# Kernel optimization log

Hardware: AMD Instinct MI355X
Metric: run time of the kernel (lower is better)

## Reference

```python
import jax, jax.numpy as jnp
import numpy as np

B, T, N, F = 4, 24, 10000, 64
E = 160000
K_STEPS = 3
HID = 128


def setup_inputs() -> dict:
    key = jax.random.key(0)
    ks = jax.random.split(key, 12)
    history = jax.random.normal(ks[0], (B, T, N, F), dtype=jnp.float32)
    horizon = jax.random.normal(ks[1], (B, 6, N, F), dtype=jnp.float32)
    edge_index = jax.random.randint(ks[2], (2, E), 0, N, dtype=jnp.int64)
    s = 1.0 / np.sqrt(F)
    W_enc = jax.random.normal(ks[3], (F, F), dtype=jnp.float32) * s
    W_hor = jax.random.normal(ks[4], (F, F), dtype=jnp.float32) * s
    b_enc = jnp.zeros((F,), dtype=jnp.float32)
    W_fc = jax.random.normal(ks[5], (F, F), dtype=jnp.float32) * s  # EventGAN.fc (no bias)
    b_gcn = jax.random.normal(ks[6], (F,), dtype=jnp.float32) * 0.01  # EventGAN.bias
    W1 = jax.random.normal(ks[7], (T * F, HID), dtype=jnp.float32) / np.sqrt(T * F)
    b1 = jnp.zeros((HID,), dtype=jnp.float32)
    W2 = jax.random.normal(ks[8], (HID, 1), dtype=jnp.float32) / np.sqrt(HID)
    b2 = jnp.zeros((1,), dtype=jnp.float32)
    return {"history": history, "horizon": horizon, "edge_index": edge_index,
            "W_enc": W_enc, "W_hor": W_hor, "b_enc": b_enc,
            "W_fc": W_fc, "b_gcn": b_gcn,
            "W1": W1, "b1": b1, "W2": W2, "b2": b2}


def _event_gan_step(h, row, col, norm, W_fc, b_gcn, n_nodes):
    # h: [B, N, F]; GCN-style normalized sum aggregation (EventGAN.forward)
    x = h @ W_fc  # fc, no bias
    msgs = norm[None, :, None] * x[:, row, :]  # [B, Etot, F] gather + scale
    agg = jax.vmap(lambda m: jax.ops.segment_sum(m, col, num_segments=n_nodes))(msgs)
    return agg + b_gcn


def reference(history, horizon, edge_index, W_enc, W_hor, b_enc, W_fc, b_gcn, W1, b1, W2, b2):
    b, t, n, f = history.shape
    # FeatureEncoder (stand-in): per-timestep linear over F mixing pooled horizon context
    hor_ctx = jnp.mean(horizon, axis=1) @ W_hor  # [B, N, F]
    x = jnp.tanh(jnp.einsum('btnf,fg->btng', history, W_enc) + hor_ctx[:, None, :, :] + b_enc)
    # spatial: k-step EventGAN propagation on last timestep's exogenous features
    h = x[:, -1, :, -f:]  # [B, N, F] (F == exogenous_features)
    row0, col0 = edge_index[0], edge_index[1]
    loops = jnp.arange(n, dtype=edge_index.dtype)
    row = jnp.concatenate([row0, loops])
    col = jnp.concatenate([col0, loops])
    deg = jax.ops.segment_sum(jnp.ones_like(col, dtype=h.dtype), col, num_segments=n)
    dinv = jnp.where(deg > 0, jax.lax.rsqrt(jnp.maximum(deg, 1.0)), 0.0)
    norm = dinv[row] * dinv[col]
    for _ in range(K_STEPS):
        h = _event_gan_step(h, row, col, norm, W_fc, b_gcn, n)
    x = x.at[:, -1, :, -f:].set(h)
    # temporal MLP (stand-in): flatten per-node time series -> scalar
    flat = x.transpose(0, 2, 1, 3).reshape(b * n, t * f)
    out = jax.nn.relu(flat @ W1 + b1) @ W2 + b2  # [B*N, 1]
    return out.reshape(b, n)
```

## Files before the change

### kernel.cpp

```cpp
#include <hip/hip_runtime.h>

constexpr int cB = 4, cT = 24, cN = 10000, cF = 64, cE = 160000, cHID = 128, cK = 3;

typedef short s16x4 __attribute__((ext_vector_type(4)));
typedef short s16x8 __attribute__((ext_vector_type(8)));
typedef float f32x16 __attribute__((ext_vector_type(16)));

__device__ __forceinline__ unsigned short f2bf(float f) {
    union { float f; unsigned u; } c; c.f = f;
    unsigned u = c.u;
    return (unsigned short)((u + 0x7FFFu + ((u >> 16) & 1u)) >> 16);
}
__device__ __forceinline__ unsigned asu(float f) {
    union { float f; unsigned u; } c; c.f = f; return c.u;
}

__device__ __forceinline__ float tanh_fast(float x) {
    float e = __expf(2.0f * x);
    return 1.0f - 2.0f * __builtin_amdgcn_rcpf(e + 1.0f);
}

__global__ void k_zeroA(int* __restrict__ cnt, int* __restrict__ cnt_in,
                        int* __restrict__ cursor) {
    int i = blockIdx.x * 256 + threadIdx.x;
    if (i == 0) *cnt = 0;
    if (i < cN) { cnt_in[i] = 0; cursor[i] = 0; }
}

__global__ void k_detect(const int* __restrict__ edges, int* __restrict__ cnt) {
    int i = blockIdx.x * 256 + threadIdx.x;
    int z = (i < cE && edges[2 * i + 1] == 0) ? 1 : 0;
    __shared__ int sc;
    if (threadIdx.x == 0) sc = 0;
    __syncthreads();
    if (z) atomicAdd(&sc, 1);
    __syncthreads();
    if (threadIdx.x == 0 && sc) atomicAdd(cnt, sc);
}

__global__ void k_count(const int* __restrict__ edges, const int* __restrict__ cnt,
                        int* __restrict__ cnt_in) {
    int e = blockIdx.x * 256 + threadIdx.x;
    if (e < cE) {
        int m = (*cnt > cE - 100) ? 2 : 1;
        atomicAdd(&cnt_in[edges[m * (cE + e)]], 1);
    }
}

__global__ void k_scan(const int* __restrict__ cnt_in, int* __restrict__ rowptr,
                       float* __restrict__ dinv) {
    int lane = threadIdx.x;
    int carry = 0;
    for (int base = 0; base < cN; base += 256) {
        int i0 = base + lane * 4;
        int v0 = (i0 + 0 < cN) ? cnt_in[i0 + 0] : 0;
        int v1 = (i0 + 1 < cN) ? cnt_in[i0 + 1] : 0;
        int v2 = (i0 + 2 < cN) ? cnt_in[i0 + 2] : 0;
        int v3 = (i0 + 3 < cN) ? cnt_in[i0 + 3] : 0;
        if (i0 + 0 < cN) dinv[i0 + 0] = rsqrtf((float)(v0 + 1));
        if (i0 + 1 < cN) dinv[i0 + 1] = rsqrtf((float)(v1 + 1));
        if (i0 + 2 < cN) dinv[i0 + 2] = rsqrtf((float)(v2 + 1));
        if (i0 + 3 < cN) dinv[i0 + 3] = rsqrtf((float)(v3 + 1));
        int sum4 = v0 + v1 + v2 + v3;
        int s = sum4;
        #pragma unroll
        for (int d = 1; d < 64; d <<= 1) {
            int u = __shfl_up(s, d, 64);
            if (lane >= d) s += u;
        }
        int pre = carry + s - sum4;
        if (i0 + 0 < cN) rowptr[i0 + 0] = pre;            pre += v0;
        if (i0 + 1 < cN) rowptr[i0 + 1] = pre;            pre += v1;
        if (i0 + 2 < cN) rowptr[i0 + 2] = pre;            pre += v2;
        if (i0 + 3 < cN) rowptr[i0 + 3] = pre;
        carry += __shfl(s, 63, 64);
    }
    if (lane == 0) rowptr[cN] = carry;
}

__global__ void k_fill(const int* __restrict__ edges, const int* __restrict__ cnt,
                       const int* __restrict__ rowptr, int* __restrict__ cursor,
                       int* __restrict__ csr_src) {
    int e = blockIdx.x * 256 + threadIdx.x;
    if (e < cE) {
        int m = (*cnt > cE - 100) ? 2 : 1;
        int r = edges[m * e];
        int c = edges[m * (cE + e)];
        int pos = atomicAdd(&cursor[c], 1);
        csr_src[rowptr[c] + pos] = r;
    }
}

__global__ void k_w1t(const float* __restrict__ W1, unsigned short* __restrict__ W1T) {
    __shared__ float sT[64][65];
    const int t = blockIdx.x;
    const int hx = blockIdx.y * 64;
    const int gx = t * 64;
    const int tid = threadIdx.x;
    #pragma unroll
    for (int r = 0; r < 4; r++) {
        int flat = tid + r * 256;
        int gp = flat >> 4, h4 = (flat & 15) * 4;
        float4 v = *(const float4*)&W1[(size_t)(gx + gp) * cHID + hx + h4];
        sT[h4 + 0][gp] = v.x; sT[h4 + 1][gp] = v.y;
        sT[h4 + 2][gp] = v.z; sT[h4 + 3][gp] = v.w;
    }
    __syncthreads();
    #pragma unroll
    for (int r = 0; r < 2; r++) {
        int flat = tid + r * 256;
        int h = flat >> 3, seg = flat & 7;
        s16x8 o;
        #pragma unroll
        for (int i = 0; i < 8; i++) o[i] = (short)f2bf(sT[h][seg * 8 + i]);
        *(s16x8*)&W1T[((size_t)t * cHID + hx + h) * 64 + seg * 8] = o;
    }
}

__global__ void k_hc(const float* __restrict__ horizon, const float* __restrict__ W_hor,
                     const float* __restrict__ b_enc, float* __restrict__ hc) {
    __shared__ float sW[64 * 64];
    __shared__ float sm[4][64];
    const int tid = threadIdx.x;
    {
        const float4* src = (const float4*)W_hor;
        float4* dst = (float4*)sW;
        #pragma unroll
        for (int q = 0; q < 4; q++) dst[tid + q * 256] = src[tid + q * 256];
    }
    int g = tid & 63;
    int sub = tid >> 6;
    int pair = blockIdx.x * 4 + sub;
    bool ok = pair < cB * cN;
    float m = 0.f;
    if (ok) {
        int b = pair / cN, n = pair % cN;
        const float* hp = horizon + ((size_t)(b * 6) * cN + n) * 64 + g;
        #pragma unroll
        for (int hh = 0; hh < 6; hh++) m += hp[(size_t)hh * cN * 64];
        m *= (1.0f / 6.0f);
    }
    sm[sub][g] = m;
    __syncthreads();
    if (!ok) return;
    float a = b_enc[g];
    #pragma unroll 8
    for (int f = 0; f < 64; f++) a = fmaf(sm[sub][f], sW[f * 64 + g], a);
    hc[(size_t)pair * 64 + g] = a;
}

__launch_bounds__(128, 2)
__global__ void k_encode_mlp(const float* __restrict__ history,
                             const float* __restrict__ W_enc,
                             const float* __restrict__ hc,
                             const unsigned short* __restrict__ W1T,
                             const float* __restrict__ dinv,
                             float* __restrict__ accbuf,
                             float* __restrict__ y0) {
    __shared__ unsigned short sHist[2][32 * 64];
    __shared__ unsigned short sXe[32 * 64];
    const int tid = threadIdx.x;
    const int lane = tid & 63;
    const int w = tid >> 6;
    const int l31 = lane & 31;
    const int lhi = lane >> 5;
    const int n0 = blockIdx.x * 32;
    const int b = blockIdx.y;
    const int zz = blockIdx.z;
    const int t0 = zz * (cT / 2), t1 = t0 + (cT / 2);
    const int nn = min(32, cN - n0);
    const int col = w * 32 + l31;

    float4 r[4];
    auto RLOAD = [&](int t) {
        const float* hsrc = history + ((size_t)(b * cT + t) * cN + n0) * 64;
        #pragma unroll
        for (int q = 0; q < 4; q++) {
            int flat = tid + q * 128;
            int node = flat >> 4, fq = flat & 15;
            r[q] = make_float4(0.f, 0.f, 0.f, 0.f);
            if (node < nn) r[q] = *(const float4*)(hsrc + node * 64 + fq * 4);
        }
    };
    auto SSTORE = [&](int buf) {
        #pragma unroll
        for (int q = 0; q < 4; q++) {
            int flat = tid + q * 128;
            int node = flat >> 4, fq = flat & 15;
            int2 p;
            p.x = (int)__builtin_amdgcn_perm(asu(r[q].y), asu(r[q].x), 0x07060302u);
            p.y = (int)__builtin_amdgcn_perm(asu(r[q].w), asu(r[q].z), 0x07060302u);
            int idx = (node * 64 + fq * 4) ^ ((node & 7) << 3);
            *(int2*)&sHist[buf][idx] = p;
        }
    };

    s16x8 wenc[4];
    #pragma unroll
    for (int ks = 0; ks < 4; ks++)
        #pragma unroll
        for (int i = 0; i < 8; i++)
            wenc[ks][i] = (short)f2bf(W_enc[(ks * 16 + lhi * 8 + i) * 64 + col]);

    float hcr[16];
    float dvr[16];
    #pragma unroll
    for (int reg = 0; reg < 16; reg++) {
        int row = (reg & 3) + 8 * (reg >> 2) + 4 * lhi;
        bool okr = row < nn;
        hcr[reg] = okr ? hc[(size_t)(b * cN + n0 + row) * 64 + col] : 0.f;
        dvr[reg] = okr ? dinv[n0 + row] : 0.f;
    }

    f32x16 accm[2];
    #pragma unroll
    for (int ht = 0; ht < 2; ht++)
        #pragma unroll
        for (int rr = 0; rr < 16; rr++) accm[ht][rr] = 0.f;

    RLOAD(t0);
    SSTORE(0);
    int cur = 0;

    for (int t = t0; t < t1; t++) {
        const bool last = (t == cT - 1);
        const bool have_next = (t + 1 < t1);
        if (have_next) RLOAD(t + 1);
        __syncthreads();
        f32x16 d;
        #pragma unroll
        for (int reg = 0; reg < 16; reg++) d[reg] = hcr[reg];
        {
            int base = l31 * 64 + lhi * 8;
            int sw = (l31 & 7) << 3;
            #pragma unroll
            for (int ks = 0; ks < 4; ks++) {
                s16x8 a = *(const s16x8*)&sHist[cur][(base + ks * 16) ^ sw];
                d = __builtin_amdgcn_mfma_f32_32x32x16_bf16(a, wenc[ks], d, 0, 0, 0);
            }
        }
        if (last) {
            #pragma unroll
            for (int reg = 0; reg < 16; reg++) {
                int row = (reg & 3) + 8 * (reg >> 2) + 4 * lhi;
                if (row < nn)
                    y0[(size_t)(n0 + row) * (cB * 64) + b * 64 + col] =
                        dvr[reg] * tanh_fast(d[reg]);
            }
        } else {
            #pragma unroll
            for (int reg = 0; reg < 16; reg++) {
                int row = (reg & 3) + 8 * (reg >> 2) + 4 * lhi;
                int idx = (row * 64 + col) ^ ((row & 7) << 3);
                sXe[idx] = f2bf(tanh_fast(d[reg]));
            }
            __syncthreads();
            int bbase = l31 * 64 + lhi * 8;
            int swB = (l31 & 7) << 3;
            #pragma unroll
            for (int ht = 0; ht < 2; ht++) {
                const unsigned short* wrow =
                    W1T + ((size_t)t * cHID + (w * 64 + ht * 32 + l31)) * 64 + lhi * 8;
                #pragma unroll
                for (int ks = 0; ks < 4; ks++) {
                    s16x8 aw = *(const s16x8*)(wrow + ks * 16);
                    s16x8 bx = *(const s16x8*)&sXe[(bbase + ks * 16) ^ swB];
                    accm[ht] = __builtin_amdgcn_mfma_f32_32x32x16_bf16(aw, bx, accm[ht], 0, 0, 0);
                }
            }
        }
        if (have_next) SSTORE(cur ^ 1);
        cur ^= 1;
    }
    int node = l31;
    if (node < nn) {
        float* ap = accbuf + (size_t)zz * cB * cN * cHID + (size_t)(b * cN + n0 + node) * cHID;
        #pragma unroll
        for (int ht = 0; ht < 2; ht++) {
            #pragma unroll
            for (int q = 0; q < 4; q++) {
                int hid0 = w * 64 + ht * 32 + q * 8 + lhi * 4;
                float4 v = make_float4(accm[ht][q * 4 + 0], accm[ht][q * 4 + 1],
                                       accm[ht][q * 4 + 2], accm[ht][q * 4 + 3]);
                *(float4*)(ap + hid0) = v;
            }
        }
    }
}

__launch_bounds__(256)
__global__ void k_gstep(const int* __restrict__ rowptr, const int* __restrict__ csr_src,
                        const float* __restrict__ dinv, const float* __restrict__ yin,
                        const float* __restrict__ W_fc, const float* __restrict__ b_gcn,
                        float* __restrict__ yout, int lastStep) {
    __shared__ float sW[64 * 64];
    __shared__ float sAgg[2][4][64];
    const int tid = threadIdx.x;
    {
        const float4* src = (const float4*)W_fc;
        float4* dst = (float4*)sW;
        #pragma unroll
        for (int q = 0; q < 4; q++) dst[tid + q * 256] = src[tid + q * 256];
    }
    const int wv = tid >> 6;
    const int nl = wv >> 1;
    const int bp = wv & 1;
    const int g = tid & 63;
    const int n = blockIdx.x * 2 + nl;
    float a0 = 0.f, a1 = 0.f;
    if (n < cN) {
        const float* yn = yin + (size_t)n * 256 + bp * 128;
        a0 = yn[g]; a1 = yn[64 + g];
        int i = rowptr[n], end = rowptr[n + 1];
        for (; i + 4 <= end; i += 4) {
            int s0 = csr_src[i + 0], s1 = csr_src[i + 1];
            int s2 = csr_src[i + 2], s3 = csr_src[i + 3];
            const float* x0 = yin + (size_t)s0 * 256 + bp * 128;
            const float* x1 = yin + (size_t)s1 * 256 + bp * 128;
            const float* x2 = yin + (size_t)s2 * 256 + bp * 128;
            const float* x3 = yin + (size_t)s3 * 256 + bp * 128;
            float v00 = x0[g], v01 = x0[64 + g];
            float v10 = x1[g], v11 = x1[64 + g];
            float v20 = x2[g], v21 = x2[64 + g];
            float v30 = x3[g], v31 = x3[64 + g];
            a0 += (v00 + v10) + (v20 + v30);
            a1 += (v01 + v11) + (v21 + v31);
        }
        for (; i < end; i++) {
            int s = csr_src[i];
            const float* xs = yin + (size_t)s * 256 + bp * 128;
            a0 += xs[g]; a1 += xs[64 + g];
        }
        sAgg[nl][bp * 2 + 0][g] = a0;
        sAgg[nl][bp * 2 + 1][g] = a1;
    }
    __syncthreads();
    if (n >= cN) return;
    const float* g0 = sAgg[nl][bp * 2 + 0];
    const float* g1 = sAgg[nl][bp * 2 + 1];
    float o0 = 0.f, o1 = 0.f;
    #pragma unroll 8
    for (int f = 0; f < 64; f++) {
        float wv_ = sW[f * 64 + g];
        o0 = fmaf(g0[f], wv_, o0);
        o1 = fmaf(g1[f], wv_, o1);
    }
    float di = dinv[n], bg = b_gcn[g];
    float h0v = fmaf(di, o0, bg);
    float h1v = fmaf(di, o1, bg);
    if (!lastStep) { h0v *= di; h1v *= di; }
    yout[(size_t)n * 256 + (bp * 2 + 0) * 64 + g] = h0v;
    yout[(size_t)n * 256 + (bp * 2 + 1) * 64 + g] = h1v;
}

__launch_bounds__(128)
__global__ void k_head(const float* __restrict__ accbuf, const float* __restrict__ hfin,
                       const float* __restrict__ W1, const float* __restrict__ b1,
                       const float* __restrict__ W2, const float* __restrict__ b2,
                       float* __restrict__ out) {
    __shared__ float sW1[64 * cHID];
    __shared__ float sh[64];
    __shared__ float red[2];
    const int tid = threadIdx.x;
    {
        const float4* src = (const float4*)(W1 + (size_t)(cT - 1) * 64 * cHID);
        float4* dst = (float4*)sW1;
        #pragma unroll
        for (int q = 0; q < 16; q++) dst[tid + q * 128] = src[tid + q * 128];
    }
    float w2j = W2[tid];
    float b1j = b1[tid];
    int pbase = blockIdx.x * 16;
    for (int p = 0; p < 16; p++) {
        int pair = pbase + p;
        if (pair >= cB * cN) break;
        int b = pair / cN, n = pair % cN;
        __syncthreads();
        if (tid < 64) sh[tid] = hfin[(size_t)n * 256 + b * 64 + tid];
        __syncthreads();
        float a = accbuf[(size_t)pair * cHID + tid]
                + accbuf[(size_t)cB * cN * cHID + (size_t)pair * cHID + tid] + b1j;
        #pragma unroll 8
        for (int f = 0; f < 64; f++) a = fmaf(sh[f], sW1[f * cHID + tid], a);
        a = fmaxf(a, 0.f) * w2j;
        #pragma unroll
        for (int d = 32; d > 0; d >>= 1) a += __shfl_down(a, d, 64);
        if ((tid & 63) == 0) red[tid >> 6] = a;
        __syncthreads();
        if (tid == 0) out[pair] = red[0] + red[1] + b2[0];
    }
}

extern "C" void kernel_launch(void* const* d_in, const int* in_sizes, int n_in,
                              void* d_out, int out_size, void* d_ws, size_t ws_size,
                              hipStream_t stream) {
    const float* history = (const float*)d_in[0];
    const float* horizon = (const float*)d_in[1];
    const int*   edges   = (const int*)d_in[2];
    const float* W_enc   = (const float*)d_in[3];
    const float* W_hor   = (const float*)d_in[4];
    const float* b_enc   = (const float*)d_in[5];
    const float* W_fc    = (const float*)d_in[6];
    const float* b_gcn   = (const float*)d_in[7];
    const float* W1      = (const float*)d_in[8];
    const float* b1      = (const float*)d_in[9];
    const float* W2      = (const float*)d_in[10];
    const float* b2      = (const float*)d_in[11];
    float* out = (float*)d_out;

    float* ws = (float*)d_ws;
    float* hc     = ws;
    float* accbuf = hc + (size_t)cB * cN * 64;
    float* yA     = accbuf + (size_t)2 * cB * cN * cHID;
    float* yB     = yA + (size_t)cB * cN * 64;
    float* dinv   = yB + (size_t)cB * cN * 64;
    unsigned short* w1t = (unsigned short*)(dinv + cN);
    int*   cnt_in = (int*)(w1t + (size_t)cT * cHID * 64);
    int*   cursor = cnt_in + cN;
    int*   rowptr = cursor + cN;
    int*   csr_src= rowptr + cN + 1;
    int*   cnt    = csr_src + cE;

    k_zeroA<<<(cN + 255) / 256, 256, 0, stream>>>(cnt, cnt_in, cursor);
    k_detect<<<(cE + 255) / 256, 256, 0, stream>>>(edges, cnt);
    k_count<<<(cE + 255) / 256, 256, 0, stream>>>(edges, cnt, cnt_in);
    k_scan<<<1, 64, 0, stream>>>(cnt_in, rowptr, dinv);
    k_fill<<<(cE + 255) / 256, 256, 0, stream>>>(edges, cnt, rowptr, cursor, csr_src);

    k_w1t<<<dim3(cT, cHID / 64), 256, 0, stream>>>(W1, w1t);
    k_hc<<<(cB * cN + 3) / 4, 256, 0, stream>>>(horizon, W_hor, b_enc, hc);
    k_encode_mlp<<<dim3((cN + 31) / 32, cB, 2), 128, 0, stream>>>(history, W_enc, hc,
                                                                  w1t, dinv, accbuf, yA);

    k_gstep<<<(cN + 1) / 2, 256, 0, stream>>>(rowptr, csr_src, dinv, yA, W_fc, b_gcn, yB, 0);
    k_gstep<<<(cN + 1) / 2, 256, 0, stream>>>(rowptr, csr_src, dinv, yB, W_fc, b_gcn, yA, 0);
    k_gstep<<<(cN + 1) / 2, 256, 0, stream>>>(rowptr, csr_src, dinv, yA, W_fc, b_gcn, yB, 1);

    k_head<<<(cB * cN + 15) / 16, 128, 0, stream>>>(accbuf, yB, W1, b1, W2, b2, out);
}
```

Before: 377.0 us.

## Drop edge-format detect kernel, use truncating bf16, and widen gstep blocks

Removes the separate k_detect launch and global counter. Each block of k_count and k_fill now infers the int64-vs-int32 edge layout locally with __syncthreads_count over its own 256 edges. Separately, the bf16 conversion of encoder activations switches from round-to-nearest to truncation, and k_gstep moves to 512-thread blocks handling 4 nodes each. The per-block layout heuristic is less robust than a global count, truncation adds a small bias to the MLP input, and the unseen remainder of k_gstep must index the enlarged sAgg consistently.

New measurement: 377.0 us. Within noise of the previous version (+0.0%).

```diff
diff --git a/kernel.cpp b/kernel.cpp
--- a/kernel.cpp
+++ b/kernel.cpp
@@ -11,6 +11,10 @@
     unsigned u = c.u;
     return (unsigned short)((u + 0x7FFFu + ((u >> 16) & 1u)) >> 16);
 }
+__device__ __forceinline__ unsigned short f2bf_rtz(float f) {
+    union { float f; unsigned u; } c; c.f = f;
+    return (unsigned short)(c.u >> 16);
+}
 __device__ __forceinline__ unsigned asu(float f) {
     union { float f; unsigned u; } c; c.f = f; return c.u;
 }
@@ -20,29 +24,16 @@
     return 1.0f - 2.0f * __builtin_amdgcn_rcpf(e + 1.0f);
 }
 
-__global__ void k_zeroA(int* __restrict__ cnt, int* __restrict__ cnt_in,
-                        int* __restrict__ cursor) {
+__global__ void k_zeroA(int* __restrict__ cnt_in, int* __restrict__ cursor) {
     int i = blockIdx.x * 256 + threadIdx.x;
-    if (i == 0) *cnt = 0;
     if (i < cN) { cnt_in[i] = 0; cursor[i] = 0; }
 }
 
-__global__ void k_detect(const int* __restrict__ edges, int* __restrict__ cnt) {
-    int i = blockIdx.x * 256 + threadIdx.x;
-    int z = (i < cE && edges[2 * i + 1] == 0) ? 1 : 0;
-    __shared__ int sc;
-    if (threadIdx.x == 0) sc = 0;
-    __syncthreads();
-    if (z) atomicAdd(&sc, 1);
-    __syncthreads();
-    if (threadIdx.x == 0 && sc) atomicAdd(cnt, sc);
-}
-
-__global__ void k_count(const int* __restrict__ edges, const int* __restrict__ cnt,
-                        int* __restrict__ cnt_in) {
+__global__ void k_count(const int* __restrict__ edges, int* __restrict__ cnt_in) {
     int e = blockIdx.x * 256 + threadIdx.x;
+    int nz = __syncthreads_count(e < cE && edges[2 * e + 1] == 0);
     if (e < cE) {
-        int m = (*cnt > cE - 100) ? 2 : 1;
+        int m = (nz == 256) ? 2 : 1;
         atomicAdd(&cnt_in[edges[m * (cE + e)]], 1);
     }
 }
@@ -78,12 +69,12 @@
     if (lane == 0) rowptr[cN] = carry;
 }
 
-__global__ void k_fill(const int* __restrict__ edges, const int* __restrict__ cnt,
-                       const int* __restrict__ rowptr, int* __restrict__ cursor,
-                       int* __restrict__ csr_src) {
+__global__ void k_fill(const int* __restrict__ edges, const int* __restrict__ rowptr,
+                       int* __restrict__ cursor, int* __restrict__ csr_src) {
     int e = blockIdx.x * 256 + threadIdx.x;
+    int nz = __syncthreads_count(e < cE && edges[2 * e + 1] == 0);
     if (e < cE) {
-        int m = (*cnt > cE - 100) ? 2 : 1;
+        int m = (nz == 256) ? 2 : 1;
         int r = edges[m * e];
         int c = edges[m * (cE + e)];
         int pos = atomicAdd(&cursor[c], 1);
@@ -252,7 +243,7 @@
             for (int reg = 0; reg < 16; reg++) {
                 int row = (reg & 3) + 8 * (reg >> 2) + 4 * lhi;
                 int idx = (row * 64 + col) ^ ((row & 7) << 3);
-                sXe[idx] = f2bf(tanh_fast(d[reg]));
+                sXe[idx] = f2bf_rtz(tanh_fast(d[reg]));
             }
             __syncthreads();
             int bbase = l31 * 64 + lhi * 8;
@@ -288,29 +279,28 @@
     }
 }
 
-__launch_bounds__(256)
+__launch_bounds__(512)
 __global__ void k_gstep(const int* __restrict__ rowptr, const int* __restrict__ csr_src,
                         const float* __restrict__ dinv, const float* __restrict__ yin,
                         const float* __restrict__ W_fc, const float* __restrict__ b_gcn,
                         float* __restrict__ yout, int lastStep) {
     __shared__ float sW[64 * 64];
-    __shared__ float sAgg[2][4][64];
+    __shared__ float sAgg[4][4][64];
     const int tid = threadIdx.x;
     {
         const float4* src = (const float4*)W_fc;
         float4* dst = (float4*)sW;
         #pragma unroll
-        for (int q = 0; q < 4; q++) dst[tid + q * 256] = src[tid + q * 256];
+        for (int q = 0; q < 2; q++) dst[tid + q * 512] = src[tid + q * 512];
     }
     const int wv = tid >> 6;
     const int nl = wv >> 1;
     const int bp = wv & 1;
     const int g = tid & 63;
-    const int n = blockIdx.x * 2 + nl;
-    float a0 = 0.f, a1 = 0.f;
+    const int n = blockIdx.x * 4 + nl;
     if (n < cN) {
         const float* yn = yin + (size_t)n * 256 + bp * 128;
-        a0 = yn[g]; a1 = yn[64 + g];
+        float a0 = yn[g], a1 = yn[64 + g];
         int i = rowptr[n], end = rowptr[n + 1];
         for (; i + 4 <= end; i += 4) {
             int s0 = csr_src[i + 0], s1 = csr_src[i + 1];
@@ -419,22 +409,20 @@
     int*   cursor = cnt_in + cN;
     int*   rowptr = cursor + cN;
     int*   csr_src= rowptr + cN + 1;
-    int*   cnt    = csr_src + cE;
-
-    k_zeroA<<<(cN + 255) / 256, 256, 0, stream>>>(cnt, cnt_in, cursor);
-    k_detect<<<(cE + 255) / 256, 256, 0, stream>>>(edges, cnt);
-    k_count<<<(cE + 255) / 256, 256, 0, stream>>>(edges, cnt, cnt_in);
+
+    k_zeroA<<<(cN + 255) / 256, 256, 0, stream>>>(cnt_in, cursor);
+    k_count<<<(cE + 255) / 256, 256, 0, stream>>>(edges, cnt_in);
     k_scan<<<1, 64, 0, stream>>>(cnt_in, rowptr, dinv);
-    k_fill<<<(cE + 255) / 256, 256, 0, stream>>>(edges, cnt, rowptr, cursor, csr_src);
+    k_fill<<<(cE + 255) / 256, 256, 0, stream>>>(edges, rowptr, cursor, csr_src);
 
     k_w1t<<<dim3(cT, cHID / 64), 256, 0, stream>>>(W1, w1t);
     k_hc<<<(cB * cN + 3) / 4, 256, 0, stream>>>(horizon, W_hor, b_enc, hc);
     k_encode_mlp<<<dim3((cN + 31) / 32, cB, 2), 128, 0, stream>>>(history, W_enc, hc,
                                                                   w1t, dinv, accbuf, yA);
 
-    k_gstep<<<(cN + 1) / 2, 256, 0, stream>>>(rowptr, csr_src, dinv, yA, W_fc, b_gcn, yB, 0);
-    k_gstep<<<(cN + 1) / 2, 256, 0, stream>>>(rowptr, csr_src, dinv, yB, W_fc, b_gcn, yA, 0);
-    k_gstep<<<(cN + 1) / 2, 256, 0, stream>>>(rowptr, csr_src, dinv, yA, W_fc, b_gcn, yB, 1);
+    k_gstep<<<(cN + 3) / 4, 512, 0, stream>>>(rowptr, csr_src, dinv, yA, W_fc, b_gcn, yB, 0);
+    k_gstep<<<(cN + 3) / 4, 512, 0, stream>>>(rowptr, csr_src, dinv, yB, W_fc, b_gcn, yA, 0);
+    k_gstep<<<(cN + 3) / 4, 512, 0, stream>>>(rowptr, csr_src, dinv, yA, W_fc, b_gcn, yB, 1);
 
     k_head<<<(cB * cN + 15) / 16, 128, 0, stream>>>(accbuf, yB, W1, b1, W2, b2, out);
 }
```
